# Optimization experiments

Hardware: AMD Instinct MI355X
Metric: run time of the kernel (lower is better)

The kernel has to match this reference:

```python
import jax, jax.numpy as jnp
import numpy as np

THETA = 10000.0


def apply_rope(x, token_position, theta=THETA):
    # x: [B, H, S, d_k] with interleaved even/odd pairs; token_position: [B, S]
    B, H, S, d_k = x.shape
    inv_freq = 1.0 / theta ** (jnp.arange(0, d_k, 2, dtype=jnp.float32) / d_k)  # [d_k/2]
    angles = token_position.astype(jnp.float32)[:, :, None] * inv_freq[None, None, :]  # [B,S,d_k/2]
    cos = jnp.cos(angles)[:, None, :, :]  # [B,1,S,d_k/2]
    sin = jnp.sin(angles)[:, None, :, :]
    xp = x.reshape(B, H, S, d_k // 2, 2)
    x_even, x_odd = xp[..., 0], xp[..., 1]
    rot_even = x_even * cos - x_odd * sin
    rot_odd = x_even * sin + x_odd * cos
    return jnp.stack([rot_even, rot_odd], axis=-1).reshape(B, H, S, d_k)


def setup_inputs() -> dict:
    key = jax.random.key(0)
    ks = jax.random.split(key, 6)
    B, S, D = 2, 2048, 2048
    x = jax.random.normal(ks[0], (B, S, D), dtype=jnp.float32)
    token_position = jnp.sort(jax.random.randint(ks[1], (B, S), 0, 2048), axis=-1).astype(jnp.int32)
    scale = 0.02
    WQ = jax.random.normal(ks[2], (D, D), dtype=jnp.float32) * scale
    WK = jax.random.normal(ks[3], (D, D), dtype=jnp.float32) * scale
    WV = jax.random.normal(ks[4], (D, D), dtype=jnp.float32) * scale
    WO = jax.random.normal(ks[5], (D, D), dtype=jnp.float32) * scale
    return {"x": x, "token_position": token_position, "WQ": WQ, "WK": WK, "WV": WV, "WO": WO}


def reference(x, token_position, WQ, WK, WV, WO):
    B, S, D = x.shape
    H = 16
    d_k = D // H

    def proj(W):
        return jnp.matmul(x, W).reshape(B, S, H, d_k).transpose(0, 2, 1, 3)  # [B,H,S,d_k]

    Q = apply_rope(proj(WQ), token_position)
    K = apply_rope(proj(WK), token_position)
    V = proj(WV)

    score = jnp.einsum('bhqd,bhkd->bhqk', Q, K) / jnp.sqrt(jnp.float32(d_k))
    causal = jnp.triu(jnp.full((S, S), -jnp.inf, dtype=jnp.float32), k=1)
    score = score + causal
    attn = jax.nn.softmax(score, axis=-1)  # stable max-sub softmax, same math
    out = jnp.einsum('bhqk,bhkd->bhqd', attn, V)
    out = out.transpose(0, 2, 1, 3).reshape(B, S, D)
    return jnp.matmul(out, WO)
```

## Files before the change

### kernel.cpp

```cpp
#include <hip/hip_runtime.h>
#include <hip/hip_bf16.h>
#include <cstdint>
#include <cstddef>

typedef unsigned short u16;
typedef __attribute__((ext_vector_type(4))) unsigned short u16x4;
typedef __attribute__((ext_vector_type(8))) unsigned short u16x8;
typedef __attribute__((ext_vector_type(8))) __bf16 bf16x8;
typedef __attribute__((ext_vector_type(4))) float f32x4;

#define MFMA16(a, b, c) __builtin_amdgcn_mfma_f32_16x16x32_bf16((a), (b), (c), 0, 0, 0)

__device__ __forceinline__ u16 f2bf(float f) {
  uint32_t u = __builtin_bit_cast(uint32_t, f);
  u += 0x7FFFu + ((u >> 16) & 1u);
  return (u16)(u >> 16);
}
__device__ __forceinline__ float bf2f(u16 h) {
  return __builtin_bit_cast(float, (uint32_t)h << 16);
}

typedef const __attribute__((address_space(1))) void gv_t;
typedef __attribute__((address_space(3))) void lv_t;
__device__ __forceinline__ void gload16(const void* g, void* l) {
  __builtin_amdgcn_global_load_lds((gv_t*)g, (lv_t*)l, 16, 0, 0);
}

__global__ void cvt_f32_to_bf16(const float* __restrict__ in, u16* __restrict__ out, int n4) {
  int i = blockIdx.x * 256 + threadIdx.x;
  if (i >= n4) return;
  float4 v = ((const float4*)in)[i];
  u16x4 o;
  o[0] = f2bf(v.x); o[1] = f2bf(v.y); o[2] = f2bf(v.z); o[3] = f2bf(v.w);
  ((u16x4*)out)[i] = o;
}

__global__ void transpose_cvt(const float* __restrict__ in, u16* __restrict__ out) {
  __shared__ float tile[32][33];
  const int bx = blockIdx.x, by = blockIdx.y;
  const int tx = threadIdx.x, ty = threadIdx.y;
#pragma unroll
  for (int i = 0; i < 32; i += 8)
    tile[ty + i][tx] = in[(size_t)(by * 32 + ty + i) * 2048 + bx * 32 + tx];
  __syncthreads();
#pragma unroll
  for (int i = 0; i < 32; i += 8)
    out[(size_t)(bx * 32 + ty + i) * 2048 + by * 32 + tx] = f2bf(tile[tx][ty + i]);
}

__global__ void vtrans(const u16* __restrict__ in, u16* __restrict__ out) {
  __shared__ u16 tile[32][34];
  const int bx = blockIdx.x, by = blockIdx.y;
  const int tx = threadIdx.x, ty = threadIdx.y;
#pragma unroll
  for (int i = 0; i < 32; i += 8)
    tile[ty + i][tx] = in[(size_t)(by * 32 + ty + i) * 2048 + bx * 32 + tx];
  __syncthreads();
#pragma unroll
  for (int i = 0; i < 32; i += 8) {
    const int c = bx * 32 + ty + i;
    const int token = by * 32 + tx;
    out[(((size_t)(token >> 11) * 16 + (c >> 7)) * 128 + (c & 127)) * 2048 + (token & 2047)] =
        tile[tx][ty + i];
  }
}

__global__ void rope2(u16* __restrict__ Q, u16* __restrict__ K, const int* __restrict__ pos) {
  const size_t idx = (size_t)blockIdx.x * 256 + threadIdx.x;
  const int i = (int)(idx & 63);
  const int s = (int)((idx >> 10) & 2047);
  const int b = (int)(idx >> 21);
  const float p = (float)pos[b * 2048 + s];
  const float freq = exp2f((float)i * -0.2076205059304601f);
  float sn, cs;
  sincosf(p * freq, &sn, &cs);
  const size_t off = ((idx >> 10) << 11) + (((idx >> 6) & 15) << 7) + 2 * i;
  {
    uint32_t* ptr = (uint32_t*)(Q + off);
    const uint32_t v = *ptr;
    const float e = bf2f((u16)(v & 0xffffu)), o = bf2f((u16)(v >> 16));
    const float sc = 0.08838834764831845f;
    *ptr = (uint32_t)f2bf((e * cs - o * sn) * sc) | ((uint32_t)f2bf((e * sn + o * cs) * sc) << 16);
  }
  {
    uint32_t* ptr = (uint32_t*)(K + off);
    const uint32_t v = *ptr;
    const float e = bf2f((u16)(v & 0xffffu)), o = bf2f((u16)(v >> 16));
    *ptr = (uint32_t)f2bf(e * cs - o * sn) | ((uint32_t)f2bf(e * sn + o * cs) << 16);
  }
}

template <int MODE>
__global__ __launch_bounds__(512, 1) void gemm8(const u16* __restrict__ A,
                                                const u16* __restrict__ Bt,
                                                void* __restrict__ Cv, int nbn) {
  constexpr int K = 2048;
  __shared__ __align__(16) u16 lds[73728];
  const int tid = threadIdx.x, lane = tid & 63;
  const int lo16 = lane & 15, hi = lane >> 4;
  const int wid = tid >> 6;
  const int wr = wid >> 1, wc = wid & 1;

  const int per = (int)gridDim.x >> 3;
  const int wg = ((int)blockIdx.x & 7) * per + ((int)blockIdx.x >> 3);
  const int bn = (wg % nbn) * 128;
  const int bm = (wg / nbn) * 256;

  const int srow = tid >> 3;
  const int scol = ((tid & 7) ^ (srow & 7)) * 8;
  const u16* Arow = A + (size_t)(bm + srow) * K + scol;
  const u16* Brow = Bt + (size_t)(bn + srow) * K + scol;
  char* dstbase = (char*)lds + tid * 16;

#define STG_A(qb_, t_, r_) \
  gload16(Arow + (size_t)(r_) * 64 * K + (t_) * 64, dstbase + (qb_) * 49152 + (r_) * 8192)
#define STG_B(qb_, t_, r_) \
  gload16(Brow + (size_t)(r_) * 64 * K + (t_) * 64, dstbase + (qb_) * 49152 + 32768 + (r_) * 8192)

  f32x4 acc[4][4];
  const f32x4 z4 = {0.f, 0.f, 0.f, 0.f};
#pragma unroll
  for (int m = 0; m < 4; ++m)
#pragma unroll
    for (int n = 0; n < 4; ++n) acc[m][n] = z4;

  const int xork = lo16 & 7;
  const int aRow = (wr * 64 + lo16) * 128;
  const int bRow = 32768 + (wc * 64 + lo16) * 128;
  const int x0 = ((hi ^ xork)) << 4;
  const int x1 = (((4 + hi) ^ xork)) << 4;

  STG_A(0, 0, 0); STG_A(0, 0, 1); STG_A(0, 0, 2); STG_A(0, 0, 3);
  STG_B(0, 0, 0); STG_B(0, 0, 1);
  STG_A(1, 1, 0); STG_A(1, 1, 1); STG_A(1, 1, 2); STG_A(1, 1, 3);
  STG_B(1, 1, 0); STG_B(1, 1, 1);

  int q = 0;
  for (int t = 0; t < 32; ++t) {
    if (t < 31) {
      asm volatile("s_waitcnt vmcnt(6)" ::: "memory");
    } else {
      asm volatile("s_waitcnt vmcnt(0)" ::: "memory");
    }
    __builtin_amdgcn_s_barrier();
    __builtin_amdgcn_sched_barrier(0);
    const char* Aq = (const char*)lds + q * 49152;
    const int q2 = (q == 0) ? 2 : q - 1;

    {
      bf16x8 a[4], b[4];
#pragma unroll
      for (int m = 0; m < 4; ++m) a[m] = *(const bf16x8*)(Aq + aRow + m * 2048 + x0);
#pragma unroll
      for (int n = 0; n < 4; ++n) b[n] = *(const bf16x8*)(Aq + bRow + n * 2048 + x0);
      if (t < 30) { STG_A(q2, t + 2, 0); STG_A(q2, t + 2, 1); STG_A(q2, t + 2, 2); }
      __builtin_amdgcn_s_setprio(1);
#pragma unroll
      for (int m = 0; m < 4; ++m)
#pragma unroll
        for (int n = 0; n < 4; ++n) acc[m][n] = MFMA16(a[m], b[n], acc[m][n]);
      __builtin_amdgcn_s_setprio(0);
    }
    __builtin_amdgcn_sched_barrier(0);
    __builtin_amdgcn_s_barrier();

    {
      bf16x8 a[4], b[4];
#pragma unroll
      for (int m = 0; m < 4; ++m) a[m] = *(const bf16x8*)(Aq + aRow + m * 2048 + x1);
#pragma unroll
      for (int n = 0; n < 4; ++n) b[n] = *(const bf16x8*)(Aq + bRow + n * 2048 + x1);
      if (t < 30) { STG_A(q2, t + 2, 3); STG_B(q2, t + 2, 0); STG_B(q2, t + 2, 1); }
      __builtin_amdgcn_s_setprio(1);
#pragma unroll
      for (int m = 0; m < 4; ++m)
#pragma unroll
        for (int n = 0; n < 4; ++n) acc[m][n] = MFMA16(a[m], b[n], acc[m][n]);
      __builtin_amdgcn_s_setprio(0);
    }
    q = (q == 2) ? 0 : q + 1;
  }
#undef STG_A
#undef STG_B

  if constexpr (MODE == 2) {
    u16* Cq = (u16*)Cv + (size_t)(bn >> 11) * 8388608;
    const int cb = (bn & 2047) + wc * 64;
#pragma unroll
    for (int m = 0; m < 4; ++m)
#pragma unroll
      for (int n = 0; n < 4; ++n)
#pragma unroll
        for (int r = 0; r < 4; ++r)
          Cq[(size_t)(bm + wr * 64 + m * 16 + hi * 4 + r) * 2048 + cb + n * 16 + lo16] =
              f2bf(acc[m][n][r]);
  } else {
    float* C = (float*)Cv;
    const int cb = bn + wc * 64;
#pragma unroll
    for (int m = 0; m < 4; ++m)
#pragma unroll
      for (int n = 0; n < 4; ++n)
#pragma unroll
        for (int r = 0; r < 4; ++r)
          C[(size_t)(bm + wr * 64 + m * 16 + hi * 4 + r) * 2048 + cb + n * 16 + lo16] =
              acc[m][n][r];
  }
}

__global__ __launch_bounds__(256, 2) void flash_attn4(const u16* __restrict__ Qb,
                                                      const u16* __restrict__ Kb,
                                                      const u16* __restrict__ VT,
                                                      u16* __restrict__ Ob) {
  constexpr int S = 2048, HD = 2048;
  const int g = (int)blockIdx.x;
  const int xcd = g & 7, slot = g >> 3;
  const int bh = xcd * 4 + (slot & 3);
  const int pairid = slot >> 2;
  const int b = bh >> 4, h = bh & 15;
  const int tid = threadIdx.x, lane = tid & 63, wid = tid >> 6;

  __shared__ u16 Ks[2][64 * 128];
  __shared__ u16 Vs[2][128 * 64];
  __shared__ u16 Ps[4][16 * 64];

  const size_t base = (size_t)b * S * HD + (size_t)h * 128;
  const u16* Qp = Qb + base;
  const u16* Kp = Kb + base;
  const u16* VTp = VT + (size_t)bh * 128 * S;
  u16* Op = Ob + base;

  const f32x4 z4 = {0.f, 0.f, 0.f, 0.f};
  const int kKv = (lane >> 4);
  const int kC16 = (lane & 15);
  const int vD = (lane >> 3);
  const int vC16 = (lane & 7);

#define STAGE(pb, kv0_)                                                                   \
  {                                                                                       \
    _Pragma("unroll") for (int c = 0; c < 4; ++c) {                                       \
      const int ch = wid * 4 + c;                                                         \
      {                                                                                   \
        const int kv = ch * 4 + kKv;                                                      \
        const int c16 = kC16 ^ (kv & 7);                                                  \
        gload16(Kp + (size_t)((kv0_) + kv) * HD + c16 * 8, (char*)Ks[pb] + ch * 1024);    \
      }                                                                                   \
      {                                                                                   \
        const int d = ch * 8 + vD;                                                        \
        const int c16 = vC16 ^ (d & 7);                                                   \
        gload16(VTp + (size_t)d * S + (kv0_) + c16 * 8, (char*)Vs[pb] + ch * 1024);       \
      }                                                                                   \
    }                                                                                     \
  }

#pragma unroll
  for (int half = 0; half < 2; ++half) {
    const int qt = half ? pairid : 31 - pairid;
    const int q0 = qt * 64;

    bf16x8 qf[4];
    {
      const int qr = q0 + wid * 16 + (lane & 15);
      const int kc = (lane >> 4) * 8;
#pragma unroll
      for (int kb = 0; kb < 4; ++kb)
        qf[kb] = *(const bf16x8*)(Qp + (size_t)qr * HD + kb * 32 + kc);
    }

    f32x4 accO[8];
#pragma unroll
    for (int d = 0; d < 8; ++d) accO[d] = z4;
    float m_r[4] = {-INFINITY, -INFINITY, -INFINITY, -INFINITY};
    float l_r[4] = {0.f, 0.f, 0.f, 0.f};

    STAGE(0, 0);
    __syncthreads();

    for (int t = 0; t <= qt; ++t) {
      const int cur = t & 1;
      const int kv0 = t * 64;
      if (t < qt) STAGE(cur ^ 1, kv0 + 64);

      const u16* Ksc = Ks[cur];
      const u16* Vsc = Vs[cur];
      f32x4 accS[4];
#pragma unroll
      for (int nb = 0; nb < 4; ++nb) accS[nb] = z4;

      __builtin_amdgcn_s_setprio(1);
#pragma unroll
      for (int nb = 0; nb < 4; ++nb) {
        const int kv = nb * 16 + (lane & 15);
#pragma unroll
        for (int kb = 0; kb < 4; ++kb) {
          const int c16 = (kb * 4 + (lane >> 4)) ^ (kv & 7);
          bf16x8 kf = *(const bf16x8*)((char*)Ksc + kv * 256 + c16 * 16);
          accS[nb] = MFMA16(qf[kb], kf, accS[nb]);
        }
      }
      __builtin_amdgcn_s_setprio(0);

      if (t == qt) {
#pragma unroll
        for (int nb = 0; nb < 4; ++nb) {
          const int kv = kv0 + nb * 16 + (lane & 15);
          const int qrow = q0 + wid * 16 + (lane >> 4) * 4;
#pragma unroll
          for (int j = 0; j < 4; ++j)
            if (kv > qrow + j) accS[nb][j] = -INFINITY;
        }
      }

      u16* Pw = &Ps[wid][0];
#pragma unroll
      for (int j = 0; j < 4; ++j) {
        float mx = fmaxf(fmaxf(accS[0][j], accS[1][j]), fmaxf(accS[2][j], accS[3][j]));
#pragma unroll
        for (int off = 1; off < 16; off <<= 1) mx = fmaxf(mx, __shfl_xor(mx, off));
        const float mn = fmaxf(m_r[j], mx);
        const float sc = __expf(m_r[j] - mn);
        m_r[j] = mn;
        float s = 0.f;
#pragma unroll
        for (int nb = 0; nb < 4; ++nb) {
          const float p = __expf(accS[nb][j] - mn);
          accS[nb][j] = p;
          s += p;
        }
#pragma unroll
        for (int off = 1; off < 16; off <<= 1) s += __shfl_xor(s, off);
        l_r[j] = l_r[j] * sc + s;
#pragma unroll
        for (int db = 0; db < 8; ++db) accO[db][j] *= sc;
        const int ql = (lane >> 4) * 4 + j;
#pragma unroll
        for (int nb = 0; nb < 4; ++nb) {
          const int col = nb * 16 + (lane & 15);
          const int byteoff = ql * 128 + ((((col >> 3) ^ (ql & 7))) << 4) + (col & 7) * 2;
          *(u16*)((char*)Pw + byteoff) = f2bf(accS[nb][j]);
        }
      }

#pragma unroll
      for (int kb2 = 0; kb2 < 2; ++kb2) {
        const int ql = lane & 15;
        const int c16a = (kb2 * 4 + (lane >> 4)) ^ (ql & 7);
        bf16x8 pa = *(const bf16x8*)((char*)Pw + ql * 128 + c16a * 16);
        __builtin_amdgcn_s_setprio(1);
#pragma unroll
        for (int db = 0; db < 8; ++db) {
          const int d = db * 16 + (lane & 15);
          const int c16 = (kb2 * 4 + (lane >> 4)) ^ (d & 7);
          bf16x8 vf = *(const bf16x8*)((char*)Vsc + d * 128 + c16 * 16);
          accO[db] = MFMA16(pa, vf, accO[db]);
        }
        __builtin_amdgcn_s_setprio(0);
      }
      __syncthreads();
    }

    float inv[4];
#pragma unroll
    for (int j = 0; j < 4; ++j) inv[j] = 1.f / l_r[j];
#pragma unroll
    for (int db = 0; db < 8; ++db)
#pragma unroll
      for (int j = 0; j < 4; ++j) {
        const int row = q0 + wid * 16 + (lane >> 4) * 4 + j;
        Op[(size_t)row * HD + db * 16 + (lane & 15)] = f2bf(accO[db][j] * inv[j]);
      }
  }
#undef STAGE
}

extern "C" void kernel_launch(void* const* d_in, const int* in_sizes, int n_in,
                              void* d_out, int out_size, void* d_ws, size_t ws_size,
                              hipStream_t stream) {
  const float* x  = (const float*)d_in[0];
  const int*   tp = (const int*)d_in[1];
  const float* WQ = (const float*)d_in[2];
  const float* WK = (const float*)d_in[3];
  const float* WV = (const float*)d_in[4];
  const float* WO = (const float*)d_in[5];

  const size_t MB = 1024 * 1024;
  if (ws_size < 112 * MB) return;
  char* ws = (char*)d_ws;
  u16* xb  = (u16*)(ws + 0 * MB);
  u16* wqt = (u16*)(ws + 16 * MB);
  u16* wkt = (u16*)(ws + 24 * MB);
  u16* wvt = (u16*)(ws + 32 * MB);
  u16* wot = (u16*)(ws + 40 * MB);
  u16* Qb  = (u16*)(ws + 48 * MB);
  u16* Kb  = (u16*)(ws + 64 * MB);
  u16* Vb  = (u16*)(ws + 80 * MB);
  u16* Obf = (u16*)(ws + 96 * MB);
  u16* VTb = xb;

  cvt_f32_to_bf16<<<8192, 256, 0, stream>>>(x, xb, 2097152);
  {
    dim3 g(64, 64), blk(32, 8);
    transpose_cvt<<<g, blk, 0, stream>>>(WQ, wqt);
    transpose_cvt<<<g, blk, 0, stream>>>(WK, wkt);
    transpose_cvt<<<g, blk, 0, stream>>>(WV, wvt);
    transpose_cvt<<<g, blk, 0, stream>>>(WO, wot);
  }
  gemm8<2><<<768, 512, 0, stream>>>(xb, wqt, (void*)Qb, 48);

  rope2<<<16384, 256, 0, stream>>>(Qb, Kb, tp);
  {
    dim3 g(64, 128), blk(32, 8);
    vtrans<<<g, blk, 0, stream>>>(Vb, VTb);
  }
  flash_attn4<<<512, 256, 0, stream>>>(Qb, Kb, VTb, Obf);

  gemm8<1><<<256, 512, 0, stream>>>(Obf, wot, d_out, 16);
}
```

Before: 287.5 us.

## Fuse RoPE into QKV GEMM epilogue, merge weight transposes, single-barrier k-loop

Removes the standalone rope2 kernel by applying rotary embedding (and the Q scale) inside the QKV GEMM epilogue, using a lane shuffle to fetch the even/odd partner. The four weight transpose launches become one launch using a z-dimension grid. The GEMM main loop now loads both k-halves of LDS fragments up front and issues all stage loads at once, dropping the mid-iteration barrier. This saves a full read/write pass over Q and K and some launch overhead, but it raises register pressure and computes sincos redundantly per element in the epilogue.

```diff
diff --git a/kernel.cpp b/kernel.cpp
--- a/kernel.cpp
+++ b/kernel.cpp
@@ -35,8 +35,13 @@
   ((u16x4*)out)[i] = o;
 }
 
-__global__ void transpose_cvt(const float* __restrict__ in, u16* __restrict__ out) {
+__global__ void transpose_cvt4(const float* __restrict__ w0, const float* __restrict__ w1,
+                               const float* __restrict__ w2, const float* __restrict__ w3,
+                               u16* __restrict__ outbase) {
   __shared__ float tile[32][33];
+  const int z = blockIdx.z;
+  const float* in = (z == 0) ? w0 : (z == 1) ? w1 : (z == 2) ? w2 : w3;
+  u16* out = outbase + (size_t)z * 4194304;
   const int bx = blockIdx.x, by = blockIdx.y;
   const int tx = threadIdx.x, ty = threadIdx.y;
 #pragma unroll
@@ -65,35 +70,11 @@
   }
 }
 
-__global__ void rope2(u16* __restrict__ Q, u16* __restrict__ K, const int* __restrict__ pos) {
-  const size_t idx = (size_t)blockIdx.x * 256 + threadIdx.x;
-  const int i = (int)(idx & 63);
-  const int s = (int)((idx >> 10) & 2047);
-  const int b = (int)(idx >> 21);
-  const float p = (float)pos[b * 2048 + s];
-  const float freq = exp2f((float)i * -0.2076205059304601f);
-  float sn, cs;
-  sincosf(p * freq, &sn, &cs);
-  const size_t off = ((idx >> 10) << 11) + (((idx >> 6) & 15) << 7) + 2 * i;
-  {
-    uint32_t* ptr = (uint32_t*)(Q + off);
-    const uint32_t v = *ptr;
-    const float e = bf2f((u16)(v & 0xffffu)), o = bf2f((u16)(v >> 16));
-    const float sc = 0.08838834764831845f;
-    *ptr = (uint32_t)f2bf((e * cs - o * sn) * sc) | ((uint32_t)f2bf((e * sn + o * cs) * sc) << 16);
-  }
-  {
-    uint32_t* ptr = (uint32_t*)(K + off);
-    const uint32_t v = *ptr;
-    const float e = bf2f((u16)(v & 0xffffu)), o = bf2f((u16)(v >> 16));
-    *ptr = (uint32_t)f2bf(e * cs - o * sn) | ((uint32_t)f2bf(e * sn + o * cs) << 16);
-  }
-}
-
 template <int MODE>
 __global__ __launch_bounds__(512, 1) void gemm8(const u16* __restrict__ A,
                                                 const u16* __restrict__ Bt,
-                                                void* __restrict__ Cv, int nbn) {
+                                                void* __restrict__ Cv,
+                                                const int* __restrict__ pos, int nbn) {
   constexpr int K = 2048;
   __shared__ __align__(16) u16 lds[73728];
   const int tid = threadIdx.x, lane = tid & 63;
@@ -147,53 +128,71 @@
     const char* Aq = (const char*)lds + q * 49152;
     const int q2 = (q == 0) ? 2 : q - 1;
 
-    {
-      bf16x8 a[4], b[4];
-#pragma unroll
-      for (int m = 0; m < 4; ++m) a[m] = *(const bf16x8*)(Aq + aRow + m * 2048 + x0);
-#pragma unroll
-      for (int n = 0; n < 4; ++n) b[n] = *(const bf16x8*)(Aq + bRow + n * 2048 + x0);
-      if (t < 30) { STG_A(q2, t + 2, 0); STG_A(q2, t + 2, 1); STG_A(q2, t + 2, 2); }
-      __builtin_amdgcn_s_setprio(1);
-#pragma unroll
-      for (int m = 0; m < 4; ++m)
-#pragma unroll
-        for (int n = 0; n < 4; ++n) acc[m][n] = MFMA16(a[m], b[n], acc[m][n]);
-      __builtin_amdgcn_s_setprio(0);
+    bf16x8 a0[4], b0[4], a1[4], b1[4];
+#pragma unroll
+    for (int m = 0; m < 4; ++m) a0[m] = *(const bf16x8*)(Aq + aRow + m * 2048 + x0);
+#pragma unroll
+    for (int n = 0; n < 4; ++n) b0[n] = *(const bf16x8*)(Aq + bRow + n * 2048 + x0);
+#pragma unroll
+    for (int m = 0; m < 4; ++m) a1[m] = *(const bf16x8*)(Aq + aRow + m * 2048 + x1);
+#pragma unroll
+    for (int n = 0; n < 4; ++n) b1[n] = *(const bf16x8*)(Aq + bRow + n * 2048 + x1);
+
+    if (t < 30) {
+      STG_A(q2, t + 2, 0); STG_A(q2, t + 2, 1); STG_A(q2, t + 2, 2); STG_A(q2, t + 2, 3);
+      STG_B(q2, t + 2, 0); STG_B(q2, t + 2, 1);
     }
-    __builtin_amdgcn_sched_barrier(0);
-    __builtin_amdgcn_s_barrier();
-
-    {
-      bf16x8 a[4], b[4];
-#pragma unroll
-      for (int m = 0; m < 4; ++m) a[m] = *(const bf16x8*)(Aq + aRow + m * 2048 + x1);
-#pragma unroll
-      for (int n = 0; n < 4; ++n) b[n] = *(const bf16x8*)(Aq + bRow + n * 2048 + x1);
-      if (t < 30) { STG_A(q2, t + 2, 3); STG_B(q2, t + 2, 0); STG_B(q2, t + 2, 1); }
-      __builtin_amdgcn_s_setprio(1);
-#pragma unroll
-      for (int m = 0; m < 4; ++m)
-#pragma unroll
-        for (int n = 0; n < 4; ++n) acc[m][n] = MFMA16(a[m], b[n], acc[m][n]);
-      __builtin_amdgcn_s_setprio(0);
-    }
+
+    __builtin_amdgcn_s_setprio(1);
+#pragma unroll
+    for (int m = 0; m < 4; ++m)
+#pragma unroll
+      for (int n = 0; n < 4; ++n) acc[m][n] = MFMA16(a0[m], b0[n], acc[m][n]);
+#pragma unroll
+    for (int m = 0; m < 4; ++m)
+#pragma unroll
+      for (int n = 0; n < 4; ++n) acc[m][n] = MFMA16(a1[m], b1[n], acc[m][n]);
+    __builtin_amdgcn_s_setprio(0);
     q = (q == 2) ? 0 : q + 1;
   }
 #undef STG_A
 #undef STG_B
 
   if constexpr (MODE == 2) {
-    u16* Cq = (u16*)Cv + (size_t)(bn >> 11) * 8388608;
+    const int sect = bn >> 11;
+    u16* Cq = (u16*)Cv + (size_t)sect * 8388608;
     const int cb = (bn & 2047) + wc * 64;
-#pragma unroll
-    for (int m = 0; m < 4; ++m)
-#pragma unroll
-      for (int n = 0; n < 4; ++n)
-#pragma unroll
-        for (int r = 0; r < 4; ++r)
-          Cq[(size_t)(bm + wr * 64 + m * 16 + hi * 4 + r) * 2048 + cb + n * 16 + lo16] =
-              f2bf(acc[m][n][r]);
+    if (sect < 2) {
+      const float qsc = (sect == 0) ? 0.08838834764831845f : 1.0f;
+#pragma unroll
+      for (int n = 0; n < 4; ++n) {
+        const int c = cb + n * 16 + lo16;
+        const float freq = exp2f((float)((c & 127) >> 1) * -0.2076205059304601f);
+        const float sgn = (c & 1) ? 1.f : -1.f;
+#pragma unroll
+        for (int m = 0; m < 4; ++m) {
+          const int row = bm + wr * 64 + m * 16 + hi * 4;
+#pragma unroll
+          for (int r = 0; r < 4; ++r) {
+            const float p = (float)pos[row + r];
+            float sn, cs;
+            sincosf(p * freq, &sn, &cs);
+            const float v = acc[m][n][r];
+            const float pv = __shfl_xor(v, 1);
+            Cq[(size_t)(row + r) * 2048 + c] = f2bf((v * cs + sgn * pv * sn) * qsc);
+          }
+        }
+      }
+    } else {
+#pragma unroll
+      for (int m = 0; m < 4; ++m)
+#pragma unroll
+        for (int n = 0; n < 4; ++n)
+#pragma unroll
+          for (int r = 0; r < 4; ++r)
+            Cq[(size_t)(bm + wr * 64 + m * 16 + hi * 4 + r) * 2048 + cb + n * 16 + lo16] =
+                f2bf(acc[m][n][r]);
+    }
   } else {
     float* C = (float*)Cv;
     const int cb = bn + wc * 64;
@@ -388,8 +387,6 @@
   char* ws = (char*)d_ws;
   u16* xb  = (u16*)(ws + 0 * MB);
   u16* wqt = (u16*)(ws + 16 * MB);
-  u16* wkt = (u16*)(ws + 24 * MB);
-  u16* wvt = (u16*)(ws + 32 * MB);
   u16* wot = (u16*)(ws + 40 * MB);
   u16* Qb  = (u16*)(ws + 48 * MB);
   u16* Kb  = (u16*)(ws + 64 * MB);
@@ -399,20 +396,16 @@
 
   cvt_f32_to_bf16<<<8192, 256, 0, stream>>>(x, xb, 2097152);
   {
-    dim3 g(64, 64), blk(32, 8);
-    transpose_cvt<<<g, blk, 0, stream>>>(WQ, wqt);
-    transpose_cvt<<<g, blk, 0, stream>>>(WK, wkt);
-    transpose_cvt<<<g, blk, 0, stream>>>(WV, wvt);
-    transpose_cvt<<<g, blk, 0, stream>>>(WO, wot);
-  }
-  gemm8<2><<<768, 512, 0, stream>>>(xb, wqt, (void*)Qb, 48);
-
-  rope2<<<16384, 256, 0, stream>>>(Qb, Kb, tp);
+    dim3 g(64, 64, 4), blk(32, 8);
+    transpose_cvt4<<<g, blk, 0, stream>>>(WQ, WK, WV, WO, wqt);
+  }
+  gemm8<2><<<768, 512, 0, stream>>>(xb, wqt, (void*)Qb, tp, 48);
+
   {
     dim3 g(64, 128), blk(32, 8);
     vtrans<<<g, blk, 0, stream>>>(Vb, VTb);
   }
   flash_attn4<<<512, 256, 0, stream>>>(Qb, Kb, VTb, Obf);
 
-  gemm8<1><<<256, 512, 0, stream>>>(Obf, wot, d_out, 16);
-}
+  gemm8<1><<<256, 512, 0, stream>>>(Obf, wot, d_out, nullptr, 16);
+}
```

Measured after the change: 333.7 us. 16.1% more time.
